# Kernel tuning notes

Hardware: AMD Instinct MI355X
Metric: run time of the kernel (lower is better)

Reference implementation:

```python
import jax, jax.numpy as jnp
import numpy as np

H = 16  # num_heads (inner_dim 1024 // default head_dim 64)
D = 64  # head_dim
EPS = 1e-5

def layernorm(x, w, b):
    mu = jnp.mean(x, axis=-1, keepdims=True)
    var = jnp.var(x, axis=-1, keepdims=True)
    return (x - mu) * jax.lax.rsqrt(var + EPS) * w + b

def attention(x, kv, wq, wk, wv, wo, bo):
    b, t, c = x.shape
    s = kv.shape[1]
    q = (x @ wq).reshape(b, t, H, D).transpose(0, 2, 1, 3)   # bhtd
    k = (kv @ wk).reshape(b, s, H, D).transpose(0, 2, 1, 3)  # bhsd
    v = (kv @ wv).reshape(b, s, H, D).transpose(0, 2, 1, 3)
    scores = jnp.einsum('bhqd,bhkd->bhqk', q, k) * (D ** -0.5)
    attn = jax.nn.softmax(scores, axis=-1)
    out = jnp.einsum('bhqk,bhkd->bhqd', attn, v)
    out = out.transpose(0, 2, 1, 3).reshape(b, t, c)
    return out @ wo + bo

def setup_inputs() -> dict:
    key = jax.random.key(0)
    ks = jax.random.split(key, 16)
    hs = 1024
    dff = 4 * hs  # 4096
    sc = lambda fan_in: 1.0 / np.sqrt(fan_in)
    inp = {
        'x': jax.random.normal(ks[0], (2, 2048, hs), jnp.float32),
        'encoder_hidden_states': jax.random.normal(ks[1], (2, 512, 64), jnp.float32),
        'ln1_w': jnp.ones((hs,), jnp.float32), 'ln1_b': jnp.zeros((hs,), jnp.float32),
        'a1_wq': jax.random.normal(ks[2], (hs, hs), jnp.float32) * sc(hs),
        'a1_wk': jax.random.normal(ks[3], (hs, hs), jnp.float32) * sc(hs),
        'a1_wv': jax.random.normal(ks[4], (hs, hs), jnp.float32) * sc(hs),
        'a1_wo': jax.random.normal(ks[5], (hs, hs), jnp.float32) * sc(hs),
        'a1_bo': jnp.zeros((hs,), jnp.float32),
        'ln2_w': jnp.ones((hs,), jnp.float32), 'ln2_b': jnp.zeros((hs,), jnp.float32),
        'a2_wq': jax.random.normal(ks[6], (hs, hs), jnp.float32) * sc(hs),
        'a2_wk': jax.random.normal(ks[7], (64, hs), jnp.float32) * sc(64),
        'a2_wv': jax.random.normal(ks[8], (64, hs), jnp.float32) * sc(64),
        'a2_wo': jax.random.normal(ks[9], (hs, hs), jnp.float32) * sc(hs),
        'a2_bo': jnp.zeros((hs,), jnp.float32),
        'ln3_w': jnp.ones((hs,), jnp.float32), 'ln3_b': jnp.zeros((hs,), jnp.float32),
        'ff_w1': jax.random.normal(ks[10], (hs, 2 * dff), jnp.float32) * sc(hs),
        'ff_b1': jnp.zeros((2 * dff,), jnp.float32),
        'ff_w2': jax.random.normal(ks[11], (dff, hs), jnp.float32) * sc(dff),
        'ff_b2': jnp.zeros((hs,), jnp.float32),
    }
    return inp

def reference(x, encoder_hidden_states, ln1_w, ln1_b, a1_wq, a1_wk, a1_wv, a1_wo, a1_bo,
              ln2_w, ln2_b, a2_wq, a2_wk, a2_wv, a2_wo, a2_bo,
              ln3_w, ln3_b, ff_w1, ff_b1, ff_w2, ff_b2):
    # self-attention sub-block
    h = layernorm(x, ln1_w, ln1_b)
    x = x + attention(h, h, a1_wq, a1_wk, a1_wv, a1_wo, a1_bo)
    # cross-attention sub-block (kv from encoder_hidden_states, dim 64)
    h = layernorm(x, ln2_w, ln2_b)
    x = x + attention(h, encoder_hidden_states, a2_wq, a2_wk, a2_wv, a2_wo, a2_bo)
    # GEGLU feed-forward sub-block
    h = layernorm(x, ln3_w, ln3_b)
    hp = h @ ff_w1 + ff_b1
    h1, h2 = jnp.split(hp, 2, axis=-1)
    h = (h1 * jax.nn.gelu(h2, approximate=False)) @ ff_w2 + ff_b2
    return x + h
```

## Files before the change

kernel.cpp:

```cpp
#include <hip/hip_runtime.h>
#include <hip/hip_bf16.h>
#include <stdint.h>

typedef unsigned short u16;
typedef __bf16 bf16x8 __attribute__((ext_vector_type(8)));
typedef float f32x4 __attribute__((ext_vector_type(4)));
typedef u16 u16x8 __attribute__((ext_vector_type(8)));
typedef u16 u16x4 __attribute__((ext_vector_type(4)));

__device__ __forceinline__ u16 f2bf(float f) {
  union { float f; uint32_t u; } v; v.f = f;
  uint32_t r = v.u + 0x7fffu + ((v.u >> 16) & 1u);
  return (u16)(r >> 16);
}
__device__ __forceinline__ float bf2f(u16 u) {
  union { uint32_t u; float f; } v; v.u = ((uint32_t)u) << 16;
  return v.f;
}
__device__ __forceinline__ uint32_t cvtpk(float a, float b) {
  uint32_t r;
  asm("v_cvt_pk_bf16_f32 %0, %1, %2" : "=v"(r) : "v"(a), "v"(b));
  return r;
}

__device__ __forceinline__ void gld16(const u16* g, u16* l) {
  __builtin_amdgcn_global_load_lds(
      (const __attribute__((address_space(1))) uint32_t*)g,
      (__attribute__((address_space(3))) uint32_t*)l, 16, 0, 0);
}

__device__ __forceinline__ void stage_half(const u16* __restrict__ gbase, int ldg,
                                           u16* lbase, int tid) {
#pragma unroll
  for (int j = 0; j < 2; ++j) {
    const int idx = j * 512 + tid;
    const int row = idx >> 3, c8 = idx & 7;
    gld16(gbase + (size_t)row * ldg + ((c8 ^ (row & 7)) << 3), lbase + idx * 8);
  }
}

struct WB {
  const float* src[6];
  u16* dst[6];
  float scale[6];
};
__global__ void wconv_b(WB wb, int K, int N) {
  const int z = blockIdx.z;
  const float* __restrict__ W = wb.src[z];
  u16* __restrict__ Wt = wb.dst[z];
  const float scale = wb.scale[z];
  __shared__ float tile[32][33];
  const int n0 = blockIdx.x * 32, k0 = blockIdx.y * 32;
  const int tx = threadIdx.x, ty = threadIdx.y;
#pragma unroll
  for (int i = 0; i < 4; ++i)
    tile[ty + 8 * i][tx] = W[(size_t)(k0 + ty + 8 * i) * N + n0 + tx];
  __syncthreads();
#pragma unroll
  for (int i = 0; i < 4; ++i)
    Wt[(size_t)(n0 + ty + 8 * i) * K + k0 + tx] = f2bf(scale * tile[tx][ty + 8 * i]);
}

__global__ void wconv_t(const float* __restrict__ W, u16* __restrict__ Wt, int K, int N) {
  __shared__ float tile[32][33];
  const int n0 = blockIdx.x * 32, k0 = blockIdx.y * 32;
  const int tx = threadIdx.x, ty = threadIdx.y;
#pragma unroll
  for (int i = 0; i < 4; ++i)
    tile[ty + 8 * i][tx] = W[(size_t)(k0 + ty + 8 * i) * N + n0 + tx];
  __syncthreads();
#pragma unroll
  for (int i = 0; i < 4; ++i)
    Wt[(size_t)(n0 + ty + 8 * i) * K + k0 + tx] = f2bf(tile[tx][ty + 8 * i]);
}

__global__ void wconv_g(const float* __restrict__ W, u16* __restrict__ Wt) {
  __shared__ float tile[32][33];
  const int n0 = blockIdx.x * 32, k0 = blockIdx.y * 32;
  const int tx = threadIdx.x, ty = threadIdx.y;
#pragma unroll
  for (int i = 0; i < 4; ++i)
    tile[ty + 8 * i][tx] = W[(size_t)(k0 + ty + 8 * i) * 8192 + n0 + tx];
  __syncthreads();
#pragma unroll
  for (int i = 0; i < 4; ++i) {
    const int n = n0 + ty + 8 * i;
    const int half = n >> 12, c = n & 4095;
    const int blk = c >> 7, cc = c & 127;
    const int wcol = cc >> 5, rem = cc & 31;
    const int sub = rem >> 4, idx = rem & 15;
    const int p = blk * 256 + wcol * 64 + (sub * 2 + half) * 16 + idx;
    Wt[(size_t)p * 1024 + k0 + tx] = f2bf(tile[tx][ty + 8 * i]);
  }
}

__global__ void cvt_bf(const float* __restrict__ in, u16* __restrict__ out, int n) {
  int i = blockIdx.x * 256 + threadIdx.x;
  if (i < n) out[i] = f2bf(in[i]);
}

__global__ __launch_bounds__(256)
void vtrans(const u16* __restrict__ V, int ldv, int hoff, u16* __restrict__ Vt, int S) {
  __shared__ u16 tile[64][72];
  const int t0 = blockIdx.x, bh = blockIdx.y;
  const int b = bh >> 4, hc = (bh & 15) * 64 + hoff;
  const int tid = threadIdx.x;
  const int r = tid >> 2, dq = (tid & 3) * 16;
  const int pos = ((r >> 5) << 5) | (((r >> 2) & 3) << 3) | (((r >> 4) & 1) << 2) | (r & 3);
  const size_t grow = ((size_t)b * S + t0 * 64 + r) * ldv + hc + dq;
  u16x8 v1 = *(const u16x8*)&V[grow];
  u16x8 v2 = *(const u16x8*)&V[grow + 8];
#pragma unroll
  for (int j = 0; j < 8; ++j) {
    tile[dq + j][pos] = v1[j];
    tile[dq + 8 + j][pos] = v2[j];
  }
  __syncthreads();
  const int d = tid >> 2, c = (tid & 3) * 16;
  u16x8 o1, o2;
#pragma unroll
  for (int j = 0; j < 8; ++j) { o1[j] = tile[d][c + j]; o2[j] = tile[d][c + 8 + j]; }
  *(u16x8*)&Vt[((size_t)bh * 64 + d) * S + t0 * 64 + c] = o1;
  *(u16x8*)&Vt[((size_t)bh * 64 + d) * S + t0 * 64 + c + 8] = o2;
}

__global__ __launch_bounds__(256)
void ln_fwd(const float* __restrict__ X, const float* __restrict__ wt,
            const float* __restrict__ bs, u16* __restrict__ Y) {
  const int row = blockIdx.x, t = threadIdx.x;
  const float4 v = *(const float4*)&X[(size_t)row * 1024 + t * 4];
  float s = v.x + v.y + v.z + v.w;
  float s2 = v.x * v.x + v.y * v.y + v.z * v.z + v.w * v.w;
#pragma unroll
  for (int off = 32; off > 0; off >>= 1) {
    s += __shfl_xor(s, off);
    s2 += __shfl_xor(s2, off);
  }
  __shared__ float rs[4], rs2[4];
  const int w = t >> 6;
  if ((t & 63) == 0) { rs[w] = s; rs2[w] = s2; }
  __syncthreads();
  s = rs[0] + rs[1] + rs[2] + rs[3];
  s2 = rs2[0] + rs2[1] + rs2[2] + rs2[3];
  const float mu = s * (1.0f / 1024.0f);
  const float var = s2 * (1.0f / 1024.0f) - mu * mu;
  const float rstd = rsqrtf(var + 1e-5f);
  const float4 wv = *(const float4*)&wt[t * 4];
  const float4 bv = *(const float4*)&bs[t * 4];
  u16x4 o;
  o[0] = f2bf((v.x - mu) * rstd * wv.x + bv.x);
  o[1] = f2bf((v.y - mu) * rstd * wv.y + bv.y);
  o[2] = f2bf((v.z - mu) * rstd * wv.z + bv.z);
  o[3] = f2bf((v.w - mu) * rstd * wv.w + bv.w);
  *(u16x4*)&Y[(size_t)row * 1024 + t * 4] = o;
}

template<int TN>
__global__ __launch_bounds__(256, 4)
void gemm_bf16(const u16* __restrict__ A, int lda, const u16* __restrict__ Bt,
               int M, int N, int K, const float* __restrict__ bias,
               const float* __restrict__ resid, float oscale,
               float* __restrict__ outF, u16* __restrict__ outB) {
  constexpr int WNV = (TN == 128) ? 2 : 1;
  constexpr int WMV = 4 / WNV;
  constexpr int WM = 128 / WMV;
  constexpr int WN = TN / WNV;
  constexpr int MI = WM / 16, NI = WN / 16;
  __shared__ __align__(16) u16 Al[128 * 64];
  __shared__ __align__(16) u16 Bl[TN * 64];
  const int tid = threadIdx.x;
  const int w = tid >> 6, l = tid & 63, lo = l & 15, g = l >> 4;
  const int gx = gridDim.x, nwg = gx * gridDim.y;
  const int lin = blockIdx.y * gx + blockIdx.x;
  const int q = nwg >> 3, r = nwg & 7;
  const int xcd = lin & 7, pos = lin >> 3;
  const int sid = (xcd < r ? xcd * (q + 1) : r * (q + 1) + (xcd - r) * q) + pos;
  const int bm = (sid % gx) * 128, bn = (sid / gx) * TN;
  const int wm = (w / WNV) * WM, wn = (w % WNV) * WN;
  const int swz = (lo & 7) << 3;
  f32x4 acc[MI][NI] = {};

  for (int k0 = 0; k0 < K; k0 += 64) {
#pragma unroll
    for (int p = 0; p < 4; ++p) {
      int idx = p * 256 + tid;
      int row = idx >> 3, c = idx & 7;
      gld16(A + (size_t)(bm + row) * lda + k0 + ((c ^ (row & 7)) << 3), &Al[idx * 8]);
    }
#pragma unroll
    for (int p = 0; p < TN / 32; ++p) {
      int idx = p * 256 + tid;
      int row = idx >> 3, c = idx & 7;
      gld16(Bt + (size_t)(bn + row) * K + k0 + ((c ^ (row & 7)) << 3), &Bl[idx * 8]);
    }
    asm volatile("s_waitcnt vmcnt(0)" ::: "memory");
    __syncthreads();
#pragma unroll
    for (int ks = 0; ks < 2; ++ks) {
      bf16x8 af[MI], bf[NI];
#pragma unroll
      for (int i = 0; i < MI; ++i)
        af[i] = *(const bf16x8*)&Al[(wm + i * 16 + lo) * 64 + ((ks * 32 + g * 8) ^ swz)];
#pragma unroll
      for (int i = 0; i < NI; ++i)
        bf[i] = *(const bf16x8*)&Bl[(wn + i * 16 + lo) * 64 + ((ks * 32 + g * 8) ^ swz)];
#pragma unroll
      for (int mi = 0; mi < MI; ++mi)
#pragma unroll
        for (int ni = 0; ni < NI; ++ni)
          acc[mi][ni] = __builtin_amdgcn_mfma_f32_16x16x32_bf16(af[mi], bf[ni], acc[mi][ni], 0, 0, 0);
    }
    __syncthreads();
  }

#pragma unroll
  for (int mi = 0; mi < MI; ++mi) {
#pragma unroll
    for (int ni = 0; ni < NI; ++ni) {
      const int col = bn + wn + ni * 16 + lo;
      const float bb = bias ? bias[col] : 0.0f;
      const int row0 = bm + wm + mi * 16 + g * 4;
#pragma unroll
      for (int rr = 0; rr < 4; ++rr) {
        const size_t off = (size_t)(row0 + rr) * N + col;
        float v = acc[mi][ni][rr] * oscale + bb;
        if (resid) v += resid[off];
        if (outF) outF[off] = v;
        else outB[off] = f2bf(v);
      }
    }
  }
}

template<int MODE>
__global__ __launch_bounds__(512, 2)
void gemm256(const u16* __restrict__ A, int lda, const u16* __restrict__ Bt,
             int M, int N, int K, const float* __restrict__ bias,
             const float* __restrict__ resid, float oscale,
             float* __restrict__ outF, u16* __restrict__ outB) {
  __shared__ __align__(16) u16 sm[65536];
  const int tid = threadIdx.x;
  const int w = tid >> 6, l = tid & 63, lo = l & 15, g = l >> 4;
  const int wrow = w >> 2, wcol = w & 3;
  const int gx = gridDim.x;
  const int nwg = gx * gridDim.y;
  const int lin = blockIdx.y * gx + blockIdx.x;
  const int q = nwg >> 3, r = nwg & 7;
  const int xcd = lin & 7, pos = lin >> 3;
  const int sid = (xcd < r ? xcd * (q + 1) : r * (q + 1) + (xcd - r) * q) + pos;
  const int bm = (sid % gx) * 256, bn = (sid / gx) * 256;

  const int NT = K >> 6;
  const int swz = (lo & 7) << 3;
  f32x4 acc[8][4] = {};

  stage_half(Bt + (size_t)bn * K, K, sm + 16384, tid);
  stage_half(Bt + (size_t)(bn + 128) * K, K, sm + 16384 + 8192, tid);
  stage_half(A + (size_t)bm * lda, lda, sm, tid);
  stage_half(A + (size_t)(bm + 128) * lda, lda, sm + 8192, tid);
  if (NT > 1) {
    stage_half(Bt + (size_t)bn * K + 64, K, sm + 32768 + 16384, tid);
    stage_half(Bt + (size_t)(bn + 128) * K + 64, K, sm + 32768 + 16384 + 8192, tid);
    stage_half(A + (size_t)bm * lda + 64, lda, sm + 32768, tid);
  }
  asm volatile("s_waitcnt vmcnt(6)" ::: "memory");
  __builtin_amdgcn_s_barrier();

  for (int t = 0; t < NT; ++t) {
    u16* Ab_ = sm + (t & 1) * 32768;
    u16* Bb_ = Ab_ + 16384;
    bf16x8 a0[4][2], a1[4][2], bfr[4][2];
#pragma unroll
    for (int mf = 0; mf < 4; ++mf) {
      const int rowi = wrow * 128 + mf * 16 + lo;
#pragma unroll
      for (int kk = 0; kk < 2; ++kk)
        a0[mf][kk] = *(const bf16x8*)&Ab_[rowi * 64 + ((kk * 32 + g * 8) ^ swz)];
    }
#pragma unroll
    for (int nf = 0; nf < 4; ++nf) {
      const int rowi = wcol * 64 + nf * 16 + lo;
#pragma unroll
      for (int kk = 0; kk < 2; ++kk)
        bfr[nf][kk] = *(const bf16x8*)&Bb_[rowi * 64 + ((kk * 32 + g * 8) ^ swz)];
    }
    if (t + 1 < NT)
      stage_half(A + (size_t)(bm + 128) * lda + (t + 1) * 64, lda,
                 sm + ((t + 1) & 1) * 32768 + 8192, tid);
    __builtin_amdgcn_s_barrier();
    __builtin_amdgcn_s_setprio(1);
#pragma unroll
    for (int mf = 0; mf < 4; ++mf)
#pragma unroll
      for (int nf = 0; nf < 2; ++nf)
#pragma unroll
        for (int kk = 0; kk < 2; ++kk)
          acc[mf][nf] = __builtin_amdgcn_mfma_f32_16x16x32_bf16(a0[mf][kk], bfr[nf][kk], acc[mf][nf], 0, 0, 0);
    __builtin_amdgcn_s_setprio(0);
    __builtin_amdgcn_s_barrier();
#pragma unroll
    for (int mf = 0; mf < 4; ++mf) {
      const int rowi = wrow * 128 + 64 + mf * 16 + lo;
#pragma unroll
      for (int kk = 0; kk < 2; ++kk)
        a1[mf][kk] = *(const bf16x8*)&Ab_[rowi * 64 + ((kk * 32 + g * 8) ^ swz)];
    }
    if (t + 2 < NT)
      stage_half(Bt + (size_t)bn * K + (t + 2) * 64, K,
                 sm + (t & 1) * 32768 + 16384, tid);
    __builtin_amdgcn_s_barrier();
    __builtin_amdgcn_s_setprio(1);
#pragma unroll
    for (int mf = 0; mf < 4; ++mf)
#pragma unroll
      for (int nf = 2; nf < 4; ++nf)
#pragma unroll
        for (int kk = 0; kk < 2; ++kk)
          acc[mf][nf] = __builtin_amdgcn_mfma_f32_16x16x32_bf16(a0[mf][kk], bfr[nf][kk], acc[mf][nf], 0, 0, 0);
    __builtin_amdgcn_s_setprio(0);
    __builtin_amdgcn_s_barrier();
    if (t + 2 < NT)
      stage_half(Bt + (size_t)(bn + 128) * K + (t + 2) * 64, K,
                 sm + (t & 1) * 32768 + 16384 + 8192, tid);
    __builtin_amdgcn_s_barrier();
    __builtin_amdgcn_s_setprio(1);
#pragma unroll
    for (int mf = 0; mf < 4; ++mf)
#pragma unroll
      for (int nf = 0; nf < 2; ++nf)
#pragma unroll
        for (int kk = 0; kk < 2; ++kk)
          acc[4 + mf][nf] = __builtin_amdgcn_mfma_f32_16x16x32_bf16(a1[mf][kk], bfr[nf][kk], acc[4 + mf][nf], 0, 0, 0);
    __builtin_amdgcn_s_setprio(0);
    __builtin_amdgcn_s_barrier();
    if (t + 2 < NT)
      stage_half(A + (size_t)bm * lda + (t + 2) * 64, lda,
                 sm + (t & 1) * 32768, tid);
    __builtin_amdgcn_s_barrier();
    __builtin_amdgcn_s_setprio(1);
#pragma unroll
    for (int mf = 0; mf < 4; ++mf)
#pragma unroll
      for (int nf = 2; nf < 4; ++nf)
#pragma unroll
        for (int kk = 0; kk < 2; ++kk)
          acc[4 + mf][nf] = __builtin_amdgcn_mfma_f32_16x16x32_bf16(a1[mf][kk], bfr[nf][kk], acc[4 + mf][nf], 0, 0, 0);
    __builtin_amdgcn_s_setprio(0);
    if (t + 2 < NT) asm volatile("s_waitcnt vmcnt(6)" ::: "memory");
    else            asm volatile("s_waitcnt vmcnt(0)" ::: "memory");
    __builtin_amdgcn_s_barrier();
  }

  if (MODE == 1) {
    const int obase = bn >> 1;
#pragma unroll
    for (int mi = 0; mi < 8; ++mi) {
#pragma unroll
      for (int sub = 0; sub < 2; ++sub) {
        const int col = obase + wcol * 32 + sub * 16 + lo;
        const float b1 = bias[col];
        const float b2 = bias[4096 + col];
#pragma unroll
        for (int rr = 0; rr < 4; ++rr) {
          const int rowi = wrow * 128 + mi * 16 + g * 4 + rr;
          const float h1 = acc[mi][sub * 2][rr] + b1;
          const float h2 = acc[mi][sub * 2 + 1][rr] + b2;
          const float ge = 0.5f * h2 * (1.0f + erff(h2 * 0.70710678118f));
          outB[(size_t)(bm + rowi) * 4096 + col] = f2bf(h1 * ge);
        }
      }
    }
    return;
  }

#pragma unroll
  for (int mi = 0; mi < 8; ++mi) {
#pragma unroll
    for (int ni = 0; ni < 4; ++ni) {
      const int col = bn + wcol * 64 + ni * 16 + lo;
      const float bb = bias ? bias[col] : 0.0f;
      const int row0 = bm + wrow * 128 + mi * 16 + g * 4;
#pragma unroll
      for (int rr = 0; rr < 4; ++rr) {
        const size_t off = (size_t)(row0 + rr) * N + col;
        float v = acc[mi][ni][rr] * oscale + bb;
        if (resid) v += resid[off];
        if (outF) outF[off] = v;
        else outB[off] = f2bf(v);
      }
    }
  }
}

__global__ __launch_bounds__(256, 4)
void attn_fwd(const u16* __restrict__ Q, int ldq, const u16* __restrict__ K, int ldk,
              const u16* __restrict__ Vt, u16* __restrict__ O, int T, int S) {
  __shared__ __align__(16) u16 Kl[2][4096];
  __shared__ __align__(16) u16 Vl[2][4096];
  const int tid = threadIdx.x, w = tid >> 6, l = tid & 63, lo = l & 15, g = l >> 4;
  const int nwg = gridDim.x * gridDim.y;
  const int n = blockIdx.y * gridDim.x + blockIdx.x;
  const int sid = (n & 7) * (nwg >> 3) + (n >> 3);
  const int qt = sid % gridDim.x, bh = sid / gridDim.x;
  const int b = bh >> 4, h = bh & 15, hc = h * 64;
  const int q0 = qt * 64 + w * 16;
  const size_t qrow = (size_t)b * T + q0;
  const size_t krow0 = (size_t)b * S;
  const size_t vrow0 = (size_t)bh * 64;

  bf16x8 qf[2];
#pragma unroll
  for (int kk = 0; kk < 2; ++kk)
    qf[kk] = *(const bf16x8*)&Q[(qrow + lo) * ldq + hc + kk * 32 + g * 8];

  f32x4 oa[4] = {};
  float m = -1e30f, lsum = 0.0f;

  const int srow = tid >> 3;
  const int scol = (((tid & 7) ^ (srow & 7)) << 3);

  const int ntile = S >> 6;
#pragma unroll
  for (int c = 0; c < 2; ++c)
    gld16(K + (krow0 + c * 32 + srow) * ldk + hc + scol, &Kl[0][c * 2048 + tid * 8]);
#pragma unroll
  for (int c = 0; c < 2; ++c)
    gld16(Vt + (vrow0 + c * 32 + srow) * S + scol, &Vl[0][c * 2048 + tid * 8]);

  for (int t0 = 0; t0 < ntile; ++t0) {
    const int cur = t0 & 1;
    if (t0 + 1 < ntile) {
      const int nxt = cur ^ 1;
#pragma unroll
      for (int c = 0; c < 2; ++c)
        gld16(K + (krow0 + (t0 + 1) * 64 + c * 32 + srow) * ldk + hc + scol,
              &Kl[nxt][c * 2048 + tid * 8]);
#pragma unroll
      for (int c = 0; c < 2; ++c)
        gld16(Vt + (vrow0 + c * 32 + srow) * S + (t0 + 1) * 64 + scol,
              &Vl[nxt][c * 2048 + tid * 8]);
      asm volatile("s_waitcnt vmcnt(4)" ::: "memory");
    } else {
      asm volatile("s_waitcnt vmcnt(0)" ::: "memory");
    }
    __builtin_amdgcn_s_barrier();

    f32x4 s[4] = {};
#pragma unroll
    for (int c = 0; c < 4; ++c)
#pragma unroll
      for (int kk = 0; kk < 2; ++kk) {
        bf16x8 kf = *(const bf16x8*)&Kl[cur][(c * 16 + lo) * 64 +
                                            ((kk * 32 + g * 8) ^ ((lo & 7) << 3))];
        s[c] = __builtin_amdgcn_mfma_f32_16x16x32_bf16(kf, qf[kk], s[c], 0, 0, 0);
      }

    float mx = fmaxf(fmaxf(fmaxf(s[0][0], s[0][1]), fmaxf(s[0][2], s[0][3])),
                     fmaxf(fmaxf(s[1][0], s[1][1]), fmaxf(s[1][2], s[1][3])));
    mx = fmaxf(mx, fmaxf(fmaxf(fmaxf(s[2][0], s[2][1]), fmaxf(s[2][2], s[2][3])),
                         fmaxf(fmaxf(s[3][0], s[3][1]), fmaxf(s[3][2], s[3][3]))));
    mx = fmaxf(mx, __shfl_xor(mx, 16));
    mx = fmaxf(mx, __shfl_xor(mx, 32));
    const float mn = fmaxf(m, mx);
    const float al = exp2f(m - mn);
    m = mn;
    float psum = 0.0f;
#pragma unroll
    for (int c = 0; c < 4; ++c)
#pragma unroll
      for (int rr = 0; rr < 4; ++rr) {
        s[c][rr] = exp2f(s[c][rr] - mn);
        psum += s[c][rr];
      }
    psum += __shfl_xor(psum, 16);
    psum += __shfl_xor(psum, 32);
    lsum = lsum * al + psum;
    f32x4 arv;
#pragma unroll
    for (int rr = 0; rr < 4; ++rr) arv[rr] = __shfl(al, 20 * g + rr);
#pragma unroll
    for (int dn = 0; dn < 4; ++dn) oa[dn] *= arv;

    union { uint32_t u[4]; bf16x8 v; } af[2];
#pragma unroll
    for (int ks = 0; ks < 2; ++ks) {
      af[ks].u[0] = cvtpk(s[2 * ks][0], s[2 * ks][1]);
      af[ks].u[1] = cvtpk(s[2 * ks][2], s[2 * ks][3]);
      af[ks].u[2] = cvtpk(s[2 * ks + 1][0], s[2 * ks + 1][1]);
      af[ks].u[3] = cvtpk(s[2 * ks + 1][2], s[2 * ks + 1][3]);
    }
#pragma unroll
    for (int dn = 0; dn < 4; ++dn)
#pragma unroll
      for (int ks = 0; ks < 2; ++ks) {
        bf16x8 vf = *(const bf16x8*)&Vl[cur][(dn * 16 + lo) * 64 +
                                            ((ks * 32 + g * 8) ^ ((lo & 7) << 3))];
        oa[dn] = __builtin_amdgcn_mfma_f32_16x16x32_bf16(af[ks].v, vf, oa[dn], 0, 0, 0);
      }
    asm volatile("s_waitcnt lgkmcnt(0)" ::: "memory");
    __builtin_amdgcn_s_barrier();
  }

  const float il = 1.0f / lsum;
  float ir[4];
#pragma unroll
  for (int rr = 0; rr < 4; ++rr) ir[rr] = __shfl(il, 20 * g + rr);
#pragma unroll
  for (int dn = 0; dn < 4; ++dn)
#pragma unroll
    for (int rr = 0; rr < 4; ++rr)
      O[(qrow + g * 4 + rr) * 1024 + hc + dn * 16 + lo] = f2bf(oa[dn][rr] * ir[rr]);
}

extern "C" void kernel_launch(void* const* d_in, const int* in_sizes, int n_in,
                              void* d_out, int out_size, void* d_ws, size_t ws_size,
                              hipStream_t stream) {
  const float* x      = (const float*)d_in[0];
  const float* enc    = (const float*)d_in[1];
  const float* ln1_w  = (const float*)d_in[2];
  const float* ln1_b  = (const float*)d_in[3];
  const float* a1_wq  = (const float*)d_in[4];
  const float* a1_wk  = (const float*)d_in[5];
  const float* a1_wv  = (const float*)d_in[6];
  const float* a1_wo  = (const float*)d_in[7];
  const float* a1_bo  = (const float*)d_in[8];
  const float* ln2_w  = (const float*)d_in[9];
  const float* ln2_b  = (const float*)d_in[10];
  const float* a2_wq  = (const float*)d_in[11];
  const float* a2_wk  = (const float*)d_in[12];
  const float* a2_wv  = (const float*)d_in[13];
  const float* a2_wo  = (const float*)d_in[14];
  const float* a2_bo  = (const float*)d_in[15];
  const float* ln3_w  = (const float*)d_in[16];
  const float* ln3_b  = (const float*)d_in[17];
  const float* ff_w1  = (const float*)d_in[18];
  const float* ff_b1  = (const float*)d_in[19];
  const float* ff_w2  = (const float*)d_in[20];
  const float* ff_b2  = (const float*)d_in[21];

  char* ws = (char*)d_ws;
  const size_t MB = 1u << 20;
  u16* wqkv1t = (u16*)(ws + 0 * MB);
  u16* wo1t   = (u16*)(ws + 6 * MB);
  u16* wq2t   = (u16*)(ws + 8 * MB);
  u16* wo2t   = (u16*)(ws + 10 * MB);
  u16* wkv2t  = (u16*)(ws + 12 * MB);
  u16* encb   = (u16*)(ws + 12 * MB + 512 * 1024);
  u16* w1t    = (u16*)(ws + 13 * MB);
  u16* w2t    = (u16*)(ws + 29 * MB);
  float* x2   = (float*)(ws + 37 * MB);
  u16* Vt1    = (u16*)(ws + 37 * MB);
  u16* Vt2    = (u16*)(ws + 45 * MB);
  u16* KVb    = (u16*)(ws + 47 * MB);
  u16* hbuf   = (u16*)(ws + 53 * MB);
  u16* qkv    = (u16*)(ws + 61 * MB);
  u16* Qb     = (u16*)(ws + 61 * MB);
  u16* Ab     = (u16*)(ws + 85 * MB);
  float* x1   = (float*)(ws + 93 * MB);
  u16* gq     = (u16*)(ws + 61 * MB);

  const float SCL = 0.125f * 1.44269504f;
  const dim3 tb(32, 8);
  {
    WB wb;
    wb.src[0] = a1_wq; wb.dst[0] = wqkv1t;               wb.scale[0] = SCL;
    wb.src[1] = a1_wk; wb.dst[1] = wqkv1t + 1024 * 1024; wb.scale[1] = 1.0f;
    wb.src[2] = a1_wv; wb.dst[2] = wqkv1t + 2048 * 1024; wb.scale[2] = 1.0f;
    wb.src[3] = a1_wo; wb.dst[3] = wo1t;                 wb.scale[3] = 1.0f;
    wb.src[4] = a2_wq; wb.dst[4] = wq2t;                 wb.scale[4] = SCL;
    wb.src[5] = a2_wo; wb.dst[5] = wo2t;                 wb.scale[5] = 1.0f;
    wconv_b<<<dim3(32, 32, 6), tb, 0, stream>>>(wb, 1024, 1024);
    WB wb2;
    wb2.src[0] = a2_wk; wb2.dst[0] = wkv2t;             wb2.scale[0] = 1.0f;
    wb2.src[1] = a2_wv; wb2.dst[1] = wkv2t + 64 * 1024; wb2.scale[1] = 1.0f;
    wb2.src[2] = a2_wk; wb2.dst[2] = wkv2t;             wb2.scale[2] = 1.0f;
    wb2.src[3] = a2_wk; wb2.dst[3] = wkv2t;             wb2.scale[3] = 1.0f;
    wb2.src[4] = a2_wk; wb2.dst[4] = wkv2t;             wb2.scale[4] = 1.0f;
    wb2.src[5] = a2_wk; wb2.dst[5] = wkv2t;             wb2.scale[5] = 1.0f;
    wconv_b<<<dim3(32, 2, 2), tb, 0, stream>>>(wb2, 64, 1024);
  }
  wconv_g<<<dim3(256, 32), tb, 0, stream>>>(ff_w1, w1t);
  wconv_t<<<dim3(32, 128), tb, 0, stream>>>(ff_w2, w2t, 4096, 1024);
  cvt_bf<<<256, 256, 0, stream>>>(enc, encb, 2 * 512 * 64);

  ln_fwd<<<4096, 256, 0, stream>>>(x, ln1_w, ln1_b, hbuf);
  gemm256<0><<<dim3(16, 12), 512, 0, stream>>>(hbuf, 1024, wqkv1t, 4096, 3072, 1024, nullptr, nullptr, 1.0f, nullptr, qkv);
  vtrans<<<dim3(32, 32), 256, 0, stream>>>(qkv, 3072, 2048, Vt1, 2048);
  attn_fwd<<<dim3(32, 32), 256, 0, stream>>>(qkv, 3072, qkv + 1024, 3072, Vt1, Ab, 2048, 2048);
  gemm_bf16<64><<<dim3(32, 16), 256, 0, stream>>>(Ab, 1024, wo1t, 4096, 1024, 1024, a1_bo, x, 1.0f, x1, nullptr);

  ln_fwd<<<4096, 256, 0, stream>>>(x1, ln2_w, ln2_b, hbuf);
  gemm_bf16<64><<<dim3(32, 16), 256, 0, stream>>>(hbuf, 1024, wq2t, 4096, 1024, 1024, nullptr, nullptr, 1.0f, nullptr, Qb);
  gemm_bf16<64><<<dim3(8, 32), 256, 0, stream>>>(encb, 64, wkv2t, 1024, 2048, 64, nullptr, nullptr, 1.0f, nullptr, KVb);
  vtrans<<<dim3(8, 32), 256, 0, stream>>>(KVb + 1024, 2048, 0, Vt2, 512);
  attn_fwd<<<dim3(32, 32), 256, 0, stream>>>(Qb, 1024, KVb, 2048, Vt2, Ab, 2048, 512);
  gemm_bf16<64><<<dim3(32, 16), 256, 0, stream>>>(Ab, 1024, wo2t, 4096, 1024, 1024, a2_bo, x1, 1.0f, x2, nullptr);

  ln_fwd<<<4096, 256, 0, stream>>>(x2, ln3_w, ln3_b, hbuf);
  gemm256<1><<<dim3(16, 32), 512, 0, stream>>>(hbuf, 1024, w1t, 4096, 8192, 1024, ff_b1, nullptr, 1.0f, nullptr, gq);
  gemm_bf16<64><<<dim3(32, 16), 256, 0, stream>>>(gq, 4096, w2t, 4096, 1024, 4096, ff_b2, x2, 1.0f, (float*)d_out, nullptr);
}
```

Before: 421.4 us.

## Software-pipeline QK^T one tile ahead of softmax and PV in attention

Restructures the flash-attention loop so the QK^T MFMAs for tile t+1 are issued in the same iteration as the softmax and PV of tile t. K loads are prefetched two tiles ahead, and V loads one tile ahead. The aim is to let matrix-core work overlap the exp/shuffle softmax math and hide latency. In exchange it holds an extra set of score accumulators in registers and adds a prologue, which may raise register pressure and lower occupancy.

```diff
diff --git a/kernel.cpp b/kernel.cpp
--- a/kernel.cpp
+++ b/kernel.cpp
@@ -418,47 +418,67 @@
 
   const int srow = tid >> 3;
   const int scol = (((tid & 7) ^ (srow & 7)) << 3);
-
   const int ntile = S >> 6;
+
 #pragma unroll
   for (int c = 0; c < 2; ++c)
     gld16(K + (krow0 + c * 32 + srow) * ldk + hc + scol, &Kl[0][c * 2048 + tid * 8]);
 #pragma unroll
   for (int c = 0; c < 2; ++c)
+    gld16(K + (krow0 + 64 + c * 32 + srow) * ldk + hc + scol, &Kl[1][c * 2048 + tid * 8]);
+#pragma unroll
+  for (int c = 0; c < 2; ++c)
     gld16(Vt + (vrow0 + c * 32 + srow) * S + scol, &Vl[0][c * 2048 + tid * 8]);
+  asm volatile("s_waitcnt vmcnt(0)" ::: "memory");
+  __builtin_amdgcn_s_barrier();
+
+  f32x4 sC[4] = {};
+#pragma unroll
+  for (int c = 0; c < 4; ++c)
+#pragma unroll
+    for (int kk = 0; kk < 2; ++kk) {
+      bf16x8 kf = *(const bf16x8*)&Kl[0][(c * 16 + lo) * 64 +
+                                        ((kk * 32 + g * 8) ^ ((lo & 7) << 3))];
+      sC[c] = __builtin_amdgcn_mfma_f32_16x16x32_bf16(kf, qf[kk], sC[c], 0, 0, 0);
+    }
+  asm volatile("s_waitcnt lgkmcnt(0)" ::: "memory");
+  __builtin_amdgcn_s_barrier();
 
   for (int t0 = 0; t0 < ntile; ++t0) {
-    const int cur = t0 & 1;
+    const int cur = t0 & 1, nxt = cur ^ 1;
+    if (t0 + 2 < ntile) {
+#pragma unroll
+      for (int c = 0; c < 2; ++c)
+        gld16(K + (krow0 + (t0 + 2) * 64 + c * 32 + srow) * ldk + hc + scol,
+              &Kl[cur][c * 2048 + tid * 8]);
+    }
     if (t0 + 1 < ntile) {
-      const int nxt = cur ^ 1;
-#pragma unroll
-      for (int c = 0; c < 2; ++c)
-        gld16(K + (krow0 + (t0 + 1) * 64 + c * 32 + srow) * ldk + hc + scol,
-              &Kl[nxt][c * 2048 + tid * 8]);
 #pragma unroll
       for (int c = 0; c < 2; ++c)
         gld16(Vt + (vrow0 + c * 32 + srow) * S + (t0 + 1) * 64 + scol,
               &Vl[nxt][c * 2048 + tid * 8]);
-      asm volatile("s_waitcnt vmcnt(4)" ::: "memory");
-    } else {
-      asm volatile("s_waitcnt vmcnt(0)" ::: "memory");
-    }
-    __builtin_amdgcn_s_barrier();
-
-    f32x4 s[4] = {};
-#pragma unroll
-    for (int c = 0; c < 4; ++c)
-#pragma unroll
-      for (int kk = 0; kk < 2; ++kk) {
-        bf16x8 kf = *(const bf16x8*)&Kl[cur][(c * 16 + lo) * 64 +
-                                            ((kk * 32 + g * 8) ^ ((lo & 7) << 3))];
-        s[c] = __builtin_amdgcn_mfma_f32_16x16x32_bf16(kf, qf[kk], s[c], 0, 0, 0);
-      }
-
-    float mx = fmaxf(fmaxf(fmaxf(s[0][0], s[0][1]), fmaxf(s[0][2], s[0][3])),
-                     fmaxf(fmaxf(s[1][0], s[1][1]), fmaxf(s[1][2], s[1][3])));
-    mx = fmaxf(mx, fmaxf(fmaxf(fmaxf(s[2][0], s[2][1]), fmaxf(s[2][2], s[2][3])),
-                         fmaxf(fmaxf(s[3][0], s[3][1]), fmaxf(s[3][2], s[3][3]))));
+    }
+    if (t0 + 2 < ntile)      asm volatile("s_waitcnt vmcnt(4)" ::: "memory");
+    else if (t0 + 1 < ntile) asm volatile("s_waitcnt vmcnt(2)" ::: "memory");
+    else                     asm volatile("s_waitcnt vmcnt(0)" ::: "memory");
+    __builtin_amdgcn_s_barrier();
+
+    f32x4 sN[4] = {};
+    if (t0 + 1 < ntile) {
+#pragma unroll
+      for (int c = 0; c < 4; ++c)
+#pragma unroll
+        for (int kk = 0; kk < 2; ++kk) {
+          bf16x8 kf = *(const bf16x8*)&Kl[nxt][(c * 16 + lo) * 64 +
+                                              ((kk * 32 + g * 8) ^ ((lo & 7) << 3))];
+          sN[c] = __builtin_amdgcn_mfma_f32_16x16x32_bf16(kf, qf[kk], sN[c], 0, 0, 0);
+        }
+    }
+
+    float mx = fmaxf(fmaxf(fmaxf(sC[0][0], sC[0][1]), fmaxf(sC[0][2], sC[0][3])),
+                     fmaxf(fmaxf(sC[1][0], sC[1][1]), fmaxf(sC[1][2], sC[1][3])));
+    mx = fmaxf(mx, fmaxf(fmaxf(fmaxf(sC[2][0], sC[2][1]), fmaxf(sC[2][2], sC[2][3])),
+                         fmaxf(fmaxf(sC[3][0], sC[3][1]), fmaxf(sC[3][2], sC[3][3]))));
     mx = fmaxf(mx, __shfl_xor(mx, 16));
     mx = fmaxf(mx, __shfl_xor(mx, 32));
     const float mn = fmaxf(m, mx);
@@ -469,8 +489,8 @@
     for (int c = 0; c < 4; ++c)
 #pragma unroll
       for (int rr = 0; rr < 4; ++rr) {
-        s[c][rr] = exp2f(s[c][rr] - mn);
-        psum += s[c][rr];
+        sC[c][rr] = exp2f(sC[c][rr] - mn);
+        psum += sC[c][rr];
       }
     psum += __shfl_xor(psum, 16);
     psum += __shfl_xor(psum, 32);
@@ -484,10 +504,10 @@
     union { uint32_t u[4]; bf16x8 v; } af[2];
 #pragma unroll
     for (int ks = 0; ks < 2; ++ks) {
-      af[ks].u[0] = cvtpk(s[2 * ks][0], s[2 * ks][1]);
-      af[ks].u[1] = cvtpk(s[2 * ks][2], s[2 * ks][3]);
-      af[ks].u[2] = cvtpk(s[2 * ks + 1][0], s[2 * ks + 1][1]);
-      af[ks].u[3] = cvtpk(s[2 * ks + 1][2], s[2 * ks + 1][3]);
+      af[ks].u[0] = cvtpk(sC[2 * ks][0], sC[2 * ks][1]);
+      af[ks].u[1] = cvtpk(sC[2 * ks][2], sC[2 * ks][3]);
+      af[ks].u[2] = cvtpk(sC[2 * ks + 1][0], sC[2 * ks + 1][1]);
+      af[ks].u[3] = cvtpk(sC[2 * ks + 1][2], sC[2 * ks + 1][3]);
     }
 #pragma unroll
     for (int dn = 0; dn < 4; ++dn)
@@ -499,6 +519,8 @@
       }
     asm volatile("s_waitcnt lgkmcnt(0)" ::: "memory");
     __builtin_amdgcn_s_barrier();
+#pragma unroll
+    for (int c = 0; c < 4; ++c) sC[c] = sN[c];
   }
 
   const float il = 1.0f / lsum;
```

New measurement: 429.9 us. 1.02x slower.

## Software-pipeline attention QK with lazy rescale and MFMA row sums; incremental GEMM pointers

Applied to the files above, without the earlier changes.

The attention kernel now computes QK^T scores for the next tile while running softmax and PV on the current tile, with K prefetched two tiles ahead and V one ahead. The running max is only updated and the output rescaled when a new max exceeds the old one by more than 8 in log2 units. Row sums are accumulated with an MFMA against a ones vector instead of shuffles, and the GEMM staging uses precomputed, incrementally advanced pointers instead of recomputing addresses. This raises register pressure, and the lazy rescale depends on fp32 headroom and on bf16 rounding of P in the row sum.

```diff
diff --git a/kernel.cpp b/kernel.cpp
--- a/kernel.cpp
+++ b/kernel.cpp
@@ -27,16 +27,6 @@
   __builtin_amdgcn_global_load_lds(
       (const __attribute__((address_space(1))) uint32_t*)g,
       (__attribute__((address_space(3))) uint32_t*)l, 16, 0, 0);
-}
-
-__device__ __forceinline__ void stage_half(const u16* __restrict__ gbase, int ldg,
-                                           u16* lbase, int tid) {
-#pragma unroll
-  for (int j = 0; j < 2; ++j) {
-    const int idx = j * 512 + tid;
-    const int row = idx >> 3, c8 = idx & 7;
-    gld16(gbase + (size_t)row * ldg + ((c8 ^ (row & 7)) << 3), lbase + idx * 8);
-  }
 }
 
 struct WB {
@@ -232,6 +222,8 @@
   }
 }
 
+#define ST2(p0, p1, dst) { gld16(p0, (dst) + tid * 8); gld16(p1, (dst) + 4096 + tid * 8); (p0) += 64; (p1) += 64; }
+
 template<int MODE>
 __global__ __launch_bounds__(512, 2)
 void gemm256(const u16* __restrict__ A, int lda, const u16* __restrict__ Bt,
@@ -254,14 +246,25 @@
   const int swz = (lo & 7) << 3;
   f32x4 acc[8][4] = {};
 
-  stage_half(Bt + (size_t)bn * K, K, sm + 16384, tid);
-  stage_half(Bt + (size_t)(bn + 128) * K, K, sm + 16384 + 8192, tid);
-  stage_half(A + (size_t)bm * lda, lda, sm, tid);
-  stage_half(A + (size_t)(bm + 128) * lda, lda, sm + 8192, tid);
+  const int sr8 = tid >> 3;
+  const int sc8 = ((tid & 7) ^ (sr8 & 7)) << 3;
+  const u16 *pA0 = A + (size_t)(bm + sr8) * lda + sc8;
+  const u16 *pA1 = A + (size_t)(bm + 64 + sr8) * lda + sc8;
+  const u16 *pA2 = A + (size_t)(bm + 128 + sr8) * lda + sc8;
+  const u16 *pA3 = A + (size_t)(bm + 192 + sr8) * lda + sc8;
+  const u16 *pB0 = Bt + (size_t)(bn + sr8) * K + sc8;
+  const u16 *pB1 = Bt + (size_t)(bn + 64 + sr8) * K + sc8;
+  const u16 *pB2 = Bt + (size_t)(bn + 128 + sr8) * K + sc8;
+  const u16 *pB3 = Bt + (size_t)(bn + 192 + sr8) * K + sc8;
+
+  ST2(pB0, pB1, sm + 16384);
+  ST2(pB2, pB3, sm + 16384 + 8192);
+  ST2(pA0, pA1, sm);
+  ST2(pA2, pA3, sm + 8192);
   if (NT > 1) {
-    stage_half(Bt + (size_t)bn * K + 64, K, sm + 32768 + 16384, tid);
-    stage_half(Bt + (size_t)(bn + 128) * K + 64, K, sm + 32768 + 16384 + 8192, tid);
-    stage_half(A + (size_t)bm * lda + 64, lda, sm + 32768, tid);
+    ST2(pB0, pB1, sm + 32768 + 16384);
+    ST2(pB2, pB3, sm + 32768 + 16384 + 8192);
+    ST2(pA0, pA1, sm + 32768);
   }
   asm volatile("s_waitcnt vmcnt(6)" ::: "memory");
   __builtin_amdgcn_s_barrier();
@@ -285,8 +288,7 @@
         bfr[nf][kk] = *(const bf16x8*)&Bb_[rowi * 64 + ((kk * 32 + g * 8) ^ swz)];
     }
     if (t + 1 < NT)
-      stage_half(A + (size_t)(bm + 128) * lda + (t + 1) * 64, lda,
-                 sm + ((t + 1) & 1) * 32768 + 8192, tid);
+      ST2(pA2, pA3, sm + ((t + 1) & 1) * 32768 + 8192);
     __builtin_amdgcn_s_barrier();
     __builtin_amdgcn_s_setprio(1);
 #pragma unroll
@@ -306,8 +308,7 @@
         a1[mf][kk] = *(const bf16x8*)&Ab_[rowi * 64 + ((kk * 32 + g * 8) ^ swz)];
     }
     if (t + 2 < NT)
-      stage_half(Bt + (size_t)bn * K + (t + 2) * 64, K,
-                 sm + (t & 1) * 32768 + 16384, tid);
+      ST2(pB0, pB1, sm + (t & 1) * 32768 + 16384);
     __builtin_amdgcn_s_barrier();
     __builtin_amdgcn_s_setprio(1);
 #pragma unroll
@@ -320,8 +321,7 @@
     __builtin_amdgcn_s_setprio(0);
     __builtin_amdgcn_s_barrier();
     if (t + 2 < NT)
-      stage_half(Bt + (size_t)(bn + 128) * K + (t + 2) * 64, K,
-                 sm + (t & 1) * 32768 + 16384 + 8192, tid);
+      ST2(pB2, pB3, sm + (t & 1) * 32768 + 16384 + 8192);
     __builtin_amdgcn_s_barrier();
     __builtin_amdgcn_s_setprio(1);
 #pragma unroll
@@ -334,8 +334,7 @@
     __builtin_amdgcn_s_setprio(0);
     __builtin_amdgcn_s_barrier();
     if (t + 2 < NT)
-      stage_half(A + (size_t)bm * lda + (t + 2) * 64, lda,
-                 sm + (t & 1) * 32768, tid);
+      ST2(pA0, pA1, sm + (t & 1) * 32768);
     __builtin_amdgcn_s_barrier();
     __builtin_amdgcn_s_setprio(1);
 #pragma unroll
@@ -391,6 +390,79 @@
     }
   }
 }
+
+#define ABODY(TT, KST, KRD, VST, VRD, SCur, SNxt)                                  \
+  {                                                                                \
+    if ((TT) + 2 < ntile) {                                                        \
+      gld16(kp0, &KST[tid * 8]);                                                   \
+      gld16(kp1, &KST[2048 + tid * 8]);                                            \
+      kp0 += kadv; kp1 += kadv;                                                    \
+    }                                                                              \
+    if ((TT) + 1 < ntile) {                                                        \
+      gld16(vp0, &VST[tid * 8]);                                                   \
+      gld16(vp1, &VST[2048 + tid * 8]);                                            \
+      vp0 += 64; vp1 += 64;                                                        \
+    }                                                                              \
+    if ((TT) + 2 < ntile)      asm volatile("s_waitcnt vmcnt(4)" ::: "memory");    \
+    else if ((TT) + 1 < ntile) asm volatile("s_waitcnt vmcnt(2)" ::: "memory");    \
+    else                       asm volatile("s_waitcnt vmcnt(0)" ::: "memory");    \
+    __builtin_amdgcn_s_barrier();                                                  \
+    if ((TT) + 1 < ntile) {                                                        \
+      _Pragma("unroll")                                                            \
+      for (int c = 0; c < 4; ++c) {                                                \
+        f32x4 zz = {};                                                             \
+        SNxt[c] = zz;                                                              \
+        _Pragma("unroll")                                                          \
+        for (int kk = 0; kk < 2; ++kk) {                                           \
+          bf16x8 kf = *(const bf16x8*)&KRD[(c * 16 + lo) * 64 +                    \
+                                           ((kk * 32 + g * 8) ^ ((lo & 7) << 3))]; \
+          SNxt[c] = __builtin_amdgcn_mfma_f32_16x16x32_bf16(kf, qf[kk], SNxt[c], 0, 0, 0); \
+        }                                                                          \
+      }                                                                            \
+    }                                                                              \
+    float mx = fmaxf(fmaxf(fmaxf(SCur[0][0], SCur[0][1]), fmaxf(SCur[0][2], SCur[0][3])),  \
+                     fmaxf(fmaxf(SCur[1][0], SCur[1][1]), fmaxf(SCur[1][2], SCur[1][3]))); \
+    mx = fmaxf(mx, fmaxf(fmaxf(fmaxf(SCur[2][0], SCur[2][1]), fmaxf(SCur[2][2], SCur[2][3])),  \
+                         fmaxf(fmaxf(SCur[3][0], SCur[3][1]), fmaxf(SCur[3][2], SCur[3][3])))); \
+    mx = fmaxf(mx, __shfl_xor(mx, 16));                                            \
+    mx = fmaxf(mx, __shfl_xor(mx, 32));                                            \
+    if (!__all(mx <= m + 8.0f)) {                                                  \
+      const float mn = fmaxf(m, mx);                                               \
+      const float al = exp2f(m - mn);                                              \
+      m = mn;                                                                      \
+      f32x4 arv;                                                                   \
+      _Pragma("unroll")                                                            \
+      for (int rr = 0; rr < 4; ++rr) arv[rr] = __shfl(al, 20 * g + rr);            \
+      _Pragma("unroll")                                                            \
+      for (int dn = 0; dn < 4; ++dn) oa[dn] *= arv;                                \
+      lrow *= arv;                                                                 \
+    }                                                                              \
+    _Pragma("unroll")                                                              \
+    for (int c = 0; c < 4; ++c)                                                    \
+      _Pragma("unroll")                                                            \
+      for (int rr = 0; rr < 4; ++rr)                                               \
+        SCur[c][rr] = exp2f(SCur[c][rr] - m);                                      \
+    union { uint32_t u[4]; bf16x8 v; } af[2];                                      \
+    _Pragma("unroll")                                                              \
+    for (int ks = 0; ks < 2; ++ks) {                                               \
+      af[ks].u[0] = cvtpk(SCur[2 * ks][0], SCur[2 * ks][1]);                       \
+      af[ks].u[1] = cvtpk(SCur[2 * ks][2], SCur[2 * ks][3]);                       \
+      af[ks].u[2] = cvtpk(SCur[2 * ks + 1][0], SCur[2 * ks + 1][1]);               \
+      af[ks].u[3] = cvtpk(SCur[2 * ks + 1][2], SCur[2 * ks + 1][3]);               \
+    }                                                                              \
+    lrow = __builtin_amdgcn_mfma_f32_16x16x32_bf16(af[0].v, onesc.v, lrow, 0, 0, 0); \
+    lrow = __builtin_amdgcn_mfma_f32_16x16x32_bf16(af[1].v, onesc.v, lrow, 0, 0, 0); \
+    _Pragma("unroll")                                                              \
+    for (int dn = 0; dn < 4; ++dn)                                                 \
+      _Pragma("unroll")                                                            \
+      for (int ks = 0; ks < 2; ++ks) {                                             \
+        bf16x8 vf = *(const bf16x8*)&VRD[(dn * 16 + lo) * 64 +                     \
+                                         ((ks * 32 + g * 8) ^ ((lo & 7) << 3))];   \
+        oa[dn] = __builtin_amdgcn_mfma_f32_16x16x32_bf16(af[ks].v, vf, oa[dn], 0, 0, 0); \
+      }                                                                            \
+    asm volatile("s_waitcnt lgkmcnt(0)" ::: "memory");                             \
+    __builtin_amdgcn_s_barrier();                                                  \
+  }
 
 __global__ __launch_bounds__(256, 4)
 void attn_fwd(const u16* __restrict__ Q, int ldq, const u16* __restrict__ K, int ldk,
@@ -413,103 +485,58 @@
   for (int kk = 0; kk < 2; ++kk)
     qf[kk] = *(const bf16x8*)&Q[(qrow + lo) * ldq + hc + kk * 32 + g * 8];
 
+  union { u16 u[8]; bf16x8 v; } onesc;
+#pragma unroll
+  for (int j = 0; j < 8; ++j) onesc.u[j] = 0x3F80;
+
   f32x4 oa[4] = {};
-  float m = -1e30f, lsum = 0.0f;
+  f32x4 lrow = {};
+  float m = -1e30f;
 
   const int srow = tid >> 3;
   const int scol = (((tid & 7) ^ (srow & 7)) << 3);
-
   const int ntile = S >> 6;
+  const size_t kadv = (size_t)64 * ldk;
+
+  const u16* kp0 = K + (krow0 + 128 + srow) * ldk + hc + scol;
+  const u16* kp1 = K + (krow0 + 160 + srow) * ldk + hc + scol;
+  const u16* vp0 = Vt + (vrow0 + srow) * S + 64 + scol;
+  const u16* vp1 = Vt + (vrow0 + 32 + srow) * S + 64 + scol;
+
 #pragma unroll
   for (int c = 0; c < 2; ++c)
     gld16(K + (krow0 + c * 32 + srow) * ldk + hc + scol, &Kl[0][c * 2048 + tid * 8]);
 #pragma unroll
   for (int c = 0; c < 2; ++c)
+    gld16(K + (krow0 + 64 + c * 32 + srow) * ldk + hc + scol, &Kl[1][c * 2048 + tid * 8]);
+#pragma unroll
+  for (int c = 0; c < 2; ++c)
     gld16(Vt + (vrow0 + c * 32 + srow) * S + scol, &Vl[0][c * 2048 + tid * 8]);
-
-  for (int t0 = 0; t0 < ntile; ++t0) {
-    const int cur = t0 & 1;
-    if (t0 + 1 < ntile) {
-      const int nxt = cur ^ 1;
-#pragma unroll
-      for (int c = 0; c < 2; ++c)
-        gld16(K + (krow0 + (t0 + 1) * 64 + c * 32 + srow) * ldk + hc + scol,
-              &Kl[nxt][c * 2048 + tid * 8]);
-#pragma unroll
-      for (int c = 0; c < 2; ++c)
-        gld16(Vt + (vrow0 + c * 32 + srow) * S + (t0 + 1) * 64 + scol,
-              &Vl[nxt][c * 2048 + tid * 8]);
-      asm volatile("s_waitcnt vmcnt(4)" ::: "memory");
-    } else {
-      asm volatile("s_waitcnt vmcnt(0)" ::: "memory");
-    }
-    __builtin_amdgcn_s_barrier();
-
-    f32x4 s[4] = {};
-#pragma unroll
-    for (int c = 0; c < 4; ++c)
-#pragma unroll
-      for (int kk = 0; kk < 2; ++kk) {
-        bf16x8 kf = *(const bf16x8*)&Kl[cur][(c * 16 + lo) * 64 +
-                                            ((kk * 32 + g * 8) ^ ((lo & 7) << 3))];
-        s[c] = __builtin_amdgcn_mfma_f32_16x16x32_bf16(kf, qf[kk], s[c], 0, 0, 0);
-      }
-
-    float mx = fmaxf(fmaxf(fmaxf(s[0][0], s[0][1]), fmaxf(s[0][2], s[0][3])),
-                     fmaxf(fmaxf(s[1][0], s[1][1]), fmaxf(s[1][2], s[1][3])));
-    mx = fmaxf(mx, fmaxf(fmaxf(fmaxf(s[2][0], s[2][1]), fmaxf(s[2][2], s[2][3])),
-                         fmaxf(fmaxf(s[3][0], s[3][1]), fmaxf(s[3][2], s[3][3]))));
-    mx = fmaxf(mx, __shfl_xor(mx, 16));
-    mx = fmaxf(mx, __shfl_xor(mx, 32));
-    const float mn = fmaxf(m, mx);
-    const float al = exp2f(m - mn);
-    m = mn;
-    float psum = 0.0f;
-#pragma unroll
-    for (int c = 0; c < 4; ++c)
-#pragma unroll
-      for (int rr = 0; rr < 4; ++rr) {
-        s[c][rr] = exp2f(s[c][rr] - mn);
-        psum += s[c][rr];
-      }
-    psum += __shfl_xor(psum, 16);
-    psum += __shfl_xor(psum, 32);
-    lsum = lsum * al + psum;
-    f32x4 arv;
-#pragma unroll
-    for (int rr = 0; rr < 4; ++rr) arv[rr] = __shfl(al, 20 * g + rr);
-#pragma unroll
-    for (int dn = 0; dn < 4; ++dn) oa[dn] *= arv;
-
-    union { uint32_t u[4]; bf16x8 v; } af[2];
-#pragma unroll
-    for (int ks = 0; ks < 2; ++ks) {
-      af[ks].u[0] = cvtpk(s[2 * ks][0], s[2 * ks][1]);
-      af[ks].u[1] = cvtpk(s[2 * ks][2], s[2 * ks][3]);
-      af[ks].u[2] = cvtpk(s[2 * ks + 1][0], s[2 * ks + 1][1]);
-      af[ks].u[3] = cvtpk(s[2 * ks + 1][2], s[2 * ks + 1][3]);
-    }
-#pragma unroll
-    for (int dn = 0; dn < 4; ++dn)
-#pragma unroll
-      for (int ks = 0; ks < 2; ++ks) {
-        bf16x8 vf = *(const bf16x8*)&Vl[cur][(dn * 16 + lo) * 64 +
-                                            ((ks * 32 + g * 8) ^ ((lo & 7) << 3))];
-        oa[dn] = __builtin_amdgcn_mfma_f32_16x16x32_bf16(af[ks].v, vf, oa[dn], 0, 0, 0);
-      }
-    asm volatile("s_waitcnt lgkmcnt(0)" ::: "memory");
-    __builtin_amdgcn_s_barrier();
-  }
-
-  const float il = 1.0f / lsum;
-  float ir[4];
-#pragma unroll
-  for (int rr = 0; rr < 4; ++rr) ir[rr] = __shfl(il, 20 * g + rr);
+  asm volatile("s_waitcnt vmcnt(0)" ::: "memory");
+  __builtin_amdgcn_s_barrier();
+
+  f32x4 sC[4] = {}, sN[4] = {};
+#pragma unroll
+  for (int c = 0; c < 4; ++c)
+#pragma unroll
+    for (int kk = 0; kk < 2; ++kk) {
+      bf16x8 kf = *(const bf16x8*)&Kl[0][(c * 16 + lo) * 64 +
+                                        ((kk * 32 + g * 8) ^ ((lo & 7) << 3))];
+      sC[c] = __builtin_amdgcn_mfma_f32_16x16x32_bf16(kf, qf[kk], sC[c], 0, 0, 0);
+    }
+  asm volatile("s_waitcnt lgkmcnt(0)" ::: "memory");
+  __builtin_amdgcn_s_barrier();
+
+  for (int t0 = 0; t0 < ntile; t0 += 2) {
+    ABODY(t0,     Kl[0], Kl[1], Vl[1], Vl[0], sC, sN)
+    ABODY(t0 + 1, Kl[1], Kl[0], Vl[0], Vl[1], sN, sC)
+  }
+
 #pragma unroll
   for (int dn = 0; dn < 4; ++dn)
 #pragma unroll
     for (int rr = 0; rr < 4; ++rr)
-      O[(qrow + g * 4 + rr) * 1024 + hc + dn * 16 + lo] = f2bf(oa[dn][rr] * ir[rr]);
+      O[(qrow + g * 4 + rr) * 1024 + hc + dn * 16 + lo] = f2bf(oa[dn][rr] / lrow[rr]);
 }
 
 extern "C" void kernel_launch(void* const* d_in, const int* in_sizes, int n_in,
```

New measurement: 409.7 us. 2.8% less time.
